# Kernel tuning notes

Hardware: AMD Instinct MI355X
Metric: run time of the kernel (lower is better)

The kernel has to match this reference:

```python
import jax, jax.numpy as jnp
import numpy as np

N_NODES = 100000

def setup_inputs() -> dict:
    key = jax.random.key(0)
    k1, k2, k3, k4 = jax.random.split(key, 4)
    feat = jax.random.normal(k1, (N_NODES, 256), dtype=jnp.float32)
    # xavier_uniform for [256,256]: bound = sqrt(6/(256+256))
    bound = float(np.sqrt(6.0 / (256 + 256)))
    weight1 = jax.random.uniform(k2, (256, 256), dtype=jnp.float32, minval=-bound, maxval=bound)
    src = jax.random.randint(k3, (1600000,), 0, N_NODES, dtype=jnp.int64)
    dst = jax.random.randint(k4, (1600000,), 0, N_NODES, dtype=jnp.int64)
    return {"feat": feat, "weight1": weight1, "src": src, "dst": dst}

def reference(feat, weight1, src, dst):
    # Per-etype copy_src + scatter-sum accumulated across etypes == one
    # segment_sum over the union of all edges (norm is computed but unused
    # in the original _apply).
    agg = jax.ops.segment_sum(feat[src], dst, num_segments=N_NODES)  # [N, d]
    h = (agg + feat) @ weight1
    h = jax.nn.relu(h)
    # F.dropout(training=False) is identity
    return h
```

## Files before the change

kernel.cpp:

```cpp
#include <hip/hip_runtime.h>

#define D 256
#define SCAN_THREADS 1024
#define CAP 32
#define MAXOVF 4096
#define BM 64

#define RN 32
#define RSH 5
#define SCAP 1024
#define PCH 8192
#define PTH 512
#define NRANGES_MAX 4096
#define SGT 256

typedef float f32x4 __attribute__((ext_vector_type(4)));
typedef short s16x8 __attribute__((ext_vector_type(8)));

__device__ inline unsigned int f2bf(float x) {
    unsigned int u = __float_as_uint(x);
    return (u + 0x7FFFu + ((u >> 16) & 1u)) >> 16;
}
__device__ inline float bflo(unsigned int u) { return __uint_as_float(u << 16); }
__device__ inline float bfhi(unsigned int u) { return __uint_as_float(u & 0xFFFF0000u); }

__global__ __launch_bounds__(256) void k_pre(const float* __restrict__ feat,
                                             unsigned short* __restrict__ featb,
                                             const float* __restrict__ W,
                                             unsigned short* __restrict__ wTs,
                                             int* __restrict__ gcur, int nz, long n8) {
    const int bid = blockIdx.x;
    const int t = threadIdx.x;
    if (bid < 256) {
        unsigned short v = (unsigned short)f2bf(W[(size_t)t * D + bid]);
        int ks = t >> 5;
        int byte = ((bid << 6) + (((t >> 3) & 3) << 4) + ((t & 7) << 1)) ^ ((bid & 7) << 4);
        *reinterpret_cast<unsigned short*>(
            reinterpret_cast<char*>(wTs) + (size_t)ks * 16384 + byte) = v;
    } else if (bid < 272) {
        int i = (bid - 256) * 256 + t;
        if (i < nz) gcur[i] = 0;
    }
    for (long i = bid * 256L + t; i < n8; i += (long)gridDim.x * 256) {
        const float4* p = reinterpret_cast<const float4*>(feat + i * 8);
        float4 a = p[0], b = p[1];
        uint4 u;
        u.x = f2bf(a.x) | (f2bf(a.y) << 16);
        u.y = f2bf(a.z) | (f2bf(a.w) << 16);
        u.z = f2bf(b.x) | (f2bf(b.y) << 16);
        u.w = f2bf(b.z) | (f2bf(b.w) << 16);
        reinterpret_cast<uint4*>(featb)[i] = u;
    }
}


__global__ void k_zero(int* __restrict__ p, int n) {
    int i = blockIdx.x * blockDim.x + threadIdx.x;
    if (i < n) p[i] = 0;
}

__global__ __launch_bounds__(256) void k_f2b(const float* __restrict__ f,
                                             unsigned short* __restrict__ fb, long n8) {
    for (long i = blockIdx.x * 256L + threadIdx.x; i < n8; i += (long)gridDim.x * 256) {
        const float4* p = reinterpret_cast<const float4*>(f + i * 8);
        float4 a = p[0], b = p[1];
        uint4 u;
        u.x = f2bf(a.x) | (f2bf(a.y) << 16);
        u.y = f2bf(a.z) | (f2bf(a.w) << 16);
        u.z = f2bf(b.x) | (f2bf(b.y) << 16);
        u.w = f2bf(b.z) | (f2bf(b.w) << 16);
        reinterpret_cast<uint4*>(fb)[i] = u;
    }
}

__global__ __launch_bounds__(256) void k_wTs(const float* __restrict__ W,
                                             unsigned short* __restrict__ wTs) {
    int col = blockIdx.x;
    int k = threadIdx.x;
    unsigned short v = (unsigned short)f2bf(W[(size_t)k * D + col]);
    int ks = k >> 5;
    int byte = ((col << 6) + (((k >> 3) & 3) << 4) + ((k & 7) << 1)) ^ ((col & 7) << 4);
    *reinterpret_cast<unsigned short*>(
        reinterpret_cast<char*>(wTs) + (size_t)ks * 16384 + byte) = v;
}

__global__ __launch_bounds__(PTH) void k_part(const int* __restrict__ src,
                                              const int* __restrict__ dst,
                                              int* __restrict__ gcur,
                                              int* __restrict__ streams,
                                              int* __restrict__ ovf,
                                              int* __restrict__ ovf_cnt,
                                              int E, int nranges) {
    __shared__ int hist[NRANGES_MAX];
    __shared__ int base[NRANGES_MAX];
    __shared__ int off[NRANGES_MAX];
    const int t = threadIdx.x;
    const long e0 = (long)blockIdx.x * PCH;
    for (int i = t; i < nranges; i += PTH) hist[i] = 0;
    __syncthreads();
    int md[PCH / PTH], ms[PCH / PTH];
    #pragma unroll
    for (int i = 0; i < PCH / PTH; ++i) {
        long e = e0 + (long)i * PTH + t;
        if (e < E) {
            md[i] = dst[e];
            ms[i] = src[e];
            atomicAdd(&hist[md[i] >> RSH], 1);
        } else {
            md[i] = -1;
        }
    }
    __syncthreads();
    for (int i = t; i < nranges; i += PTH) {
        int h = hist[i];
        base[i] = h ? atomicAdd(&gcur[i], h) : 0;
        off[i] = 0;
    }
    __syncthreads();
    #pragma unroll
    for (int i = 0; i < PCH / PTH; ++i) {
        if (md[i] >= 0) {
            int r = md[i] >> RSH;
            int p = base[r] + atomicAdd(&off[r], 1);
            if (p < SCAP) {
                streams[(size_t)r * SCAP + p] = (ms[i] << RSH) | (md[i] & (RN - 1));
            } else {
                int o = atomicAdd(ovf_cnt, 1);
                if (o < MAXOVF) { ovf[2 * o] = ms[i]; ovf[2 * o + 1] = md[i]; }
            }
        }
    }
}

__global__ __launch_bounds__(SGT) void k_sg(const unsigned short* __restrict__ featb,
                                            const int* __restrict__ gcur,
                                            const int* __restrict__ streams,
                                            const int* __restrict__ ovf,
                                            const int* __restrict__ ovf_cnt,
                                            unsigned short* __restrict__ aggb, int N) {
    __shared__ int hist[RN], basei[RN], off[RN], scn[RN];
    __shared__ int elist[SCAP];
    const int r = blockIdx.x;
    const int t = threadIdx.x;
    const int node0 = r << RSH;
    int cnt = gcur[r];
    if (cnt > SCAP) cnt = SCAP;
    if (t < RN) { hist[t] = 0; off[t] = 0; }
    __syncthreads();
    int ent[SCAP / SGT];
    #pragma unroll
    for (int i = 0; i < SCAP / SGT; ++i) {
        int p = t + i * SGT;
        if (p < cnt) {
            ent[i] = streams[(size_t)r * SCAP + p];
            atomicAdd(&hist[ent[i] & (RN - 1)], 1);
        } else {
            ent[i] = -1;
        }
    }
    __syncthreads();
    if (t < RN) scn[t] = hist[t];
    __syncthreads();
    for (int st = 1; st < RN; st <<= 1) {
        int v = 0;
        if (t < RN && t >= st) v = scn[t - st];
        __syncthreads();
        if (t < RN) scn[t] += v;
        __syncthreads();
    }
    if (t < RN) basei[t] = scn[t] - hist[t];
    __syncthreads();
    #pragma unroll
    for (int i = 0; i < SCAP / SGT; ++i) {
        if (ent[i] >= 0) {
            int ln_ = ent[i] & (RN - 1);
            int p = basei[ln_] + atomicAdd(&off[ln_], 1);
            elist[p] = ent[i] >> RSH;
        }
    }
    __syncthreads();
    int ovfn = *ovf_cnt;
    if (ovfn > MAXOVF) ovfn = MAXOVF;
    const int wv = t >> 6;
    const int l = t & 63;
    for (int k = 0; k < RN / 4; ++k) {
        int ln_ = wv * (RN / 4) + k;
        int node = node0 + ln_;
        if (node >= N) continue;
        int cb = hist[ln_];
        int bb = basei[ln_];
        uint2 u = reinterpret_cast<const uint2*>(featb + (size_t)node * D)[l];
        float4 acc;
        acc.x = bflo(u.x); acc.y = bfhi(u.x); acc.z = bflo(u.y); acc.w = bfhi(u.y);
        int j = 0;
        for (; j + 16 <= cb; j += 16) {
            int s[16];
            #pragma unroll
            for (int q = 0; q < 16; ++q) s[q] = elist[bb + j + q];
            uint2 v[16];
            #pragma unroll
            for (int q = 0; q < 16; ++q)
                v[q] = reinterpret_cast<const uint2*>(featb + (size_t)s[q] * D)[l];
            #pragma unroll
            for (int q = 0; q < 16; ++q) {
                acc.x += bflo(v[q].x); acc.y += bfhi(v[q].x);
                acc.z += bflo(v[q].y); acc.w += bfhi(v[q].y);
            }
        }
        for (; j + 8 <= cb; j += 8) {
            int s[8];
            #pragma unroll
            for (int q = 0; q < 8; ++q) s[q] = elist[bb + j + q];
            uint2 v[8];
            #pragma unroll
            for (int q = 0; q < 8; ++q)
                v[q] = reinterpret_cast<const uint2*>(featb + (size_t)s[q] * D)[l];
            #pragma unroll
            for (int q = 0; q < 8; ++q) {
                acc.x += bflo(v[q].x); acc.y += bfhi(v[q].x);
                acc.z += bflo(v[q].y); acc.w += bfhi(v[q].y);
            }
        }
        for (; j < cb; ++j) {
            uint2 v = reinterpret_cast<const uint2*>(featb + (size_t)elist[bb + j] * D)[l];
            acc.x += bflo(v.x); acc.y += bfhi(v.x);
            acc.z += bflo(v.y); acc.w += bfhi(v.y);
        }
        if (ovfn > 0) {
            for (int e = 0; e < ovfn; ++e) {
                if (ovf[2 * e + 1] == node) {
                    uint2 v = reinterpret_cast<const uint2*>(featb + (size_t)ovf[2 * e] * D)[l];
                    acc.x += bflo(v.x); acc.y += bfhi(v.x);
                    acc.z += bflo(v.y); acc.w += bfhi(v.y);
                }
            }
        }
        uint2 w;
        w.x = f2bf(acc.x) | (f2bf(acc.y) << 16);
        w.y = f2bf(acc.z) | (f2bf(acc.w) << 16);
        unsigned short* rowp = aggb + (size_t)node * D;
        int us = (l * 4) ^ ((node & 7) << 3);
        *reinterpret_cast<uint2*>(rowp + us) = w;
    }
}

__global__ void k_fillcap(const int* __restrict__ src, const int* __restrict__ dst,
                          int* __restrict__ counts, int* __restrict__ buckets,
                          int* __restrict__ ovf, int* __restrict__ ovf_cnt, int E) {
    for (int e = blockIdx.x * blockDim.x + threadIdx.x; e < E;
         e += gridDim.x * blockDim.x) {
        int d = dst[e];
        int pos = atomicAdd(&counts[d], 1);
        if (pos < CAP) {
            buckets[(size_t)d * CAP + pos] = src[e];
        } else {
            int o = atomicAdd(ovf_cnt, 1);
            if (o < MAXOVF) {
                ovf[2 * o + 0] = src[e];
                ovf[2 * o + 1] = d;
            }
        }
    }
}


#define GAT_BODY(LOAD, ACCUM)                                                  \
    int j = 0;                                                                 \
    for (; j + 16 <= cnt; j += 16) {                                           \
        int s[16];                                                             \
        _Pragma("unroll") for (int q = 0; q < 16; ++q) s[q] = bk[j + q];       \
        LOAD(16)                                                               \
        ACCUM(16)                                                              \
    }                                                                          \
    for (; j + 8 <= cnt; j += 8) {                                             \
        int s[8];                                                              \
        _Pragma("unroll") for (int q = 0; q < 8; ++q) s[q] = bk[j + q];        \
        LOAD(8)                                                                \
        ACCUM(8)                                                               \
    }

__global__ __launch_bounds__(256) void g_bf_aggb(const unsigned short* __restrict__ fb,
                                                 const int* __restrict__ counts,
                                                 const int* __restrict__ buckets,
                                                 const int* __restrict__ ovf,
                                                 const int* __restrict__ ovf_cnt,
                                                 unsigned short* __restrict__ aggb, int N) {
    int node = (int)((blockIdx.x * (long)blockDim.x + threadIdx.x) >> 6);
    int ln = threadIdx.x & 63;
    if (node >= N) return;
    int cnt_raw = counts[node];
    int cnt = cnt_raw > CAP ? CAP : cnt_raw;
    const int* bk = buckets + (size_t)node * CAP;
    uint2 u = reinterpret_cast<const uint2*>(fb + (size_t)node * D)[ln];
    float4 acc;
    acc.x = bflo(u.x); acc.y = bfhi(u.x); acc.z = bflo(u.y); acc.w = bfhi(u.y);
#define BLOAD(W_)                                                              \
    uint2 v[W_];                                                               \
    _Pragma("unroll") for (int q = 0; q < W_; ++q)                             \
        v[q] = reinterpret_cast<const uint2*>(fb + (size_t)s[q] * D)[ln];
#define BACC(W_)                                                               \
    _Pragma("unroll") for (int q = 0; q < W_; ++q) {                           \
        acc.x += bflo(v[q].x); acc.y += bfhi(v[q].x);                          \
        acc.z += bflo(v[q].y); acc.w += bfhi(v[q].y);                          \
    }
    GAT_BODY(BLOAD, BACC)
    for (; j < cnt; ++j) {
        uint2 v = reinterpret_cast<const uint2*>(fb + (size_t)bk[j] * D)[ln];
        acc.x += bflo(v.x); acc.y += bfhi(v.x);
        acc.z += bflo(v.y); acc.w += bfhi(v.y);
    }
    if (cnt_raw > CAP) {
        int m = *ovf_cnt;
        if (m > MAXOVF) m = MAXOVF;
        for (int e = 0; e < m; ++e) {
            if (ovf[2 * e + 1] == node) {
                uint2 v = reinterpret_cast<const uint2*>(fb + (size_t)ovf[2 * e] * D)[ln];
                acc.x += bflo(v.x); acc.y += bfhi(v.x);
                acc.z += bflo(v.y); acc.w += bfhi(v.y);
            }
        }
    }
    uint2 w;
    w.x = f2bf(acc.x) | (f2bf(acc.y) << 16);
    w.y = f2bf(acc.z) | (f2bf(acc.w) << 16);
    unsigned short* rowp = aggb + (size_t)node * D;
    int us = (ln * 4) ^ ((node & 7) << 3);
    *reinterpret_cast<uint2*>(rowp + us) = w;
}

__global__ __launch_bounds__(256) void g_f32_out(const float* __restrict__ feat,
                                                 const int* __restrict__ counts,
                                                 const int* __restrict__ buckets,
                                                 const int* __restrict__ ovf,
                                                 const int* __restrict__ ovf_cnt,
                                                 float* __restrict__ out, int N) {
    int node = (int)((blockIdx.x * (long)blockDim.x + threadIdx.x) >> 6);
    int ln = threadIdx.x & 63;
    if (node >= N) return;
    int cnt_raw = counts[node];
    int cnt = cnt_raw > CAP ? CAP : cnt_raw;
    const int* bk = buckets + (size_t)node * CAP;
    float4 acc = reinterpret_cast<const float4*>(feat + (size_t)node * D)[ln];
#define FLOAD(W_)                                                              \
    float4 v[W_];                                                              \
    _Pragma("unroll") for (int q = 0; q < W_; ++q)                             \
        v[q] = reinterpret_cast<const float4*>(feat + (size_t)s[q] * D)[ln];
#define FACC(W_)                                                               \
    _Pragma("unroll") for (int q = 0; q < W_; ++q) {                           \
        acc.x += v[q].x; acc.y += v[q].y; acc.z += v[q].z; acc.w += v[q].w;    \
    }
    GAT_BODY(FLOAD, FACC)
    for (; j < cnt; ++j) {
        float4 v = reinterpret_cast<const float4*>(feat + (size_t)bk[j] * D)[ln];
        acc.x += v.x; acc.y += v.y; acc.z += v.z; acc.w += v.w;
    }
    if (cnt_raw > CAP) {
        int m = *ovf_cnt;
        if (m > MAXOVF) m = MAXOVF;
        for (int e = 0; e < m; ++e) {
            if (ovf[2 * e + 1] == node) {
                float4 v = reinterpret_cast<const float4*>(feat + (size_t)ovf[2 * e] * D)[ln];
                acc.x += v.x; acc.y += v.y; acc.z += v.z; acc.w += v.w;
            }
        }
    }
    reinterpret_cast<float4*>(out + (size_t)node * D)[ln] = acc;
}


__global__ __launch_bounds__(256) void gc_copy(const float* __restrict__ feat,
                                               float* __restrict__ agg, long n4) {
    long i = (long)blockIdx.x * blockDim.x + threadIdx.x;
    if (i < n4)
        reinterpret_cast<float4*>(agg)[i] = reinterpret_cast<const float4*>(feat)[i];
}

__global__ __launch_bounds__(256) void gc_scatter(const float* __restrict__ feat,
                                                  const int* __restrict__ src,
                                                  const int* __restrict__ dst,
                                                  float* __restrict__ agg, int n_edges) {
    int wave = (int)((blockIdx.x * (long)blockDim.x + threadIdx.x) >> 6);
    int lane = threadIdx.x & 63;
    if (wave >= n_edges) return;
    int s = src[wave];
    int d = dst[wave];
    const float4 v = reinterpret_cast<const float4*>(feat + (size_t)s * D)[lane];
    float* p = agg + (size_t)d * D + (size_t)lane * 4;
    atomicAdd(p + 0, v.x);
    atomicAdd(p + 1, v.y);
    atomicAdd(p + 2, v.z);
    atomicAdd(p + 3, v.w);
}


__device__ inline void gload16(const char* g, const unsigned char* lds) {
    __builtin_amdgcn_global_load_lds(
        (const __attribute__((address_space(1))) void*)g,
        (__attribute__((address_space(3))) void*)lds, 16, 0, 0);
}

__global__ __launch_bounds__(256) void gemm_mfma_b(const unsigned short* __restrict__ aggb,
                                                   const unsigned short* __restrict__ wTs,
                                                   float* __restrict__ out, int n_rows) {
    __shared__ __align__(16) unsigned char s_a[BM * 512];
    __shared__ __align__(16) unsigned char s_b[16384];
    const int t = threadIdx.x;
    const int row0 = blockIdx.x * BM;
    const int wv = t >> 6;
    const int l = t & 63;
    const char* wb = reinterpret_cast<const char*>(wTs);

    const char* gbase = reinterpret_cast<const char*>(aggb) + (size_t)row0 * 512;
    #pragma unroll
    for (int q = 0; q < 8; ++q) {
        int off = wv * 8192 + q * 1024;
        gload16(gbase + off + l * 16, s_a + off);
    }
    #pragma unroll
    for (int i = 0; i < 4; ++i) {
        int off = wv * 4096 + i * 1024;
        gload16(wb + off + l * 16, s_b + off);
    }
    __syncthreads();

    f32x4 acc[16];
    #pragma unroll
    for (int ct = 0; ct < 16; ++ct) acc[ct] = (f32x4){0.f, 0.f, 0.f, 0.f};

    const int lr = wv * 16 + (l & 15);
    const int g = l >> 4;
    for (int ks = 0; ks < 8; ++ks) {
        const int kb = ks * 32 + g * 8;
        const int ab = (lr * 512 + kb * 2) ^ ((lr & 7) << 4);
        s16x8 af = *reinterpret_cast<const s16x8*>(s_a + ab);
        #pragma unroll
        for (int ct = 0; ct < 16; ++ct) {
            int col = ct * 16 + (l & 15);
            int bb = (col * 64 + g * 16) ^ ((col & 7) << 4);
            s16x8 bf = *reinterpret_cast<const s16x8*>(s_b + bb);
            acc[ct] = __builtin_amdgcn_mfma_f32_16x16x32_bf16(af, bf, acc[ct], 0, 0, 0);
        }
        __syncthreads();
        if (ks < 7) {
            #pragma unroll
            for (int i = 0; i < 4; ++i) {
                int off = wv * 4096 + i * 1024;
                gload16(wb + (size_t)(ks + 1) * 16384 + off + l * 16, s_b + off);
            }
            __syncthreads();
        }
    }

    const int rbase = row0 + wv * 16 + (l >> 4) * 4;
    const int cb = l & 15;
    #pragma unroll
    for (int ct = 0; ct < 16; ++ct) {
        #pragma unroll
        for (int r = 0; r < 4; ++r) {
            int row = rbase + r;
            if (row < n_rows)
                out[(size_t)row * D + ct * 16 + cb] = fmaxf(acc[ct][r], 0.f);
        }
    }
}

__global__ __launch_bounds__(256) void gemm_mfma(const unsigned short* __restrict__ wTs,
                                                 float* __restrict__ out, int n_rows) {
    __shared__ __align__(16) unsigned char s_a[BM * 512];
    __shared__ __align__(16) unsigned char s_b[16384];
    const int t = threadIdx.x;
    const int row0 = blockIdx.x * BM;
    const int wv = t >> 6;
    const int l = t & 63;
    const char* wb = reinterpret_cast<const char*>(wTs);

    #pragma unroll
    for (int i = 0; i < 4; ++i) {
        int off = wv * 4096 + i * 1024;
        gload16(wb + off + l * 16, s_b + off);
    }
    #pragma unroll
    for (int i = 0; i < 16; ++i) {
        int f4 = t + 256 * i;
        int row = f4 >> 6;
        int kc = f4 & 63;
        int grow = row0 + row;
        if (grow >= n_rows) grow = n_rows - 1;
        float4 v = *reinterpret_cast<const float4*>(out + (size_t)grow * D + kc * 4);
        uint2 u;
        u.x = f2bf(v.x) | (f2bf(v.y) << 16);
        u.y = f2bf(v.z) | (f2bf(v.w) << 16);
        int byte = (row * 512 + kc * 8) ^ ((row & 7) << 4);
        *reinterpret_cast<uint2*>(s_a + byte) = u;
    }
    __syncthreads();

    f32x4 acc[16];
    #pragma unroll
    for (int ct = 0; ct < 16; ++ct) acc[ct] = (f32x4){0.f, 0.f, 0.f, 0.f};

    const int lr = wv * 16 + (l & 15);
    const int g = l >> 4;
    for (int ks = 0; ks < 8; ++ks) {
        const int kb = ks * 32 + g * 8;
        const int ab = (lr * 512 + kb * 2) ^ ((lr & 7) << 4);
        s16x8 af = *reinterpret_cast<const s16x8*>(s_a + ab);
        #pragma unroll
        for (int ct = 0; ct < 16; ++ct) {
            int col = ct * 16 + (l & 15);
            int bb = (col * 64 + g * 16) ^ ((col & 7) << 4);
            s16x8 bf = *reinterpret_cast<const s16x8*>(s_b + bb);
            acc[ct] = __builtin_amdgcn_mfma_f32_16x16x32_bf16(af, bf, acc[ct], 0, 0, 0);
        }
        __syncthreads();
        if (ks < 7) {
            #pragma unroll
            for (int i = 0; i < 4; ++i) {
                int off = wv * 4096 + i * 1024;
                gload16(wb + (size_t)(ks + 1) * 16384 + off + l * 16, s_b + off);
            }
            __syncthreads();
        }
    }

    const int rbase = row0 + wv * 16 + (l >> 4) * 4;
    const int cb = l & 15;
    #pragma unroll
    for (int ct = 0; ct < 16; ++ct) {
        #pragma unroll
        for (int r = 0; r < 4; ++r) {
            int row = rbase + r;
            if (row < n_rows)
                out[(size_t)row * D + ct * 16 + cb] = fmaxf(acc[ct][r], 0.f);
        }
    }
}

__global__ __launch_bounds__(256) void gemm_relu(const float* __restrict__ Wm,
                                                 float* __restrict__ out, int n_rows) {
    __shared__ float s_a[32][D];
    const int row0 = blockIdx.x * 32;
    const int c = threadIdx.x;
    {
        const float4* gsrc = reinterpret_cast<const float4*>(out + (size_t)row0 * D);
        float4* ldst = reinterpret_cast<float4*>(&s_a[0][0]);
        #pragma unroll
        for (int i = 0; i < 8; ++i)
            ldst[threadIdx.x + i * 256] = gsrc[threadIdx.x + i * 256];
    }
    __syncthreads();
    float acc[32];
    #pragma unroll
    for (int r = 0; r < 32; ++r) acc[r] = 0.f;
    #pragma unroll 4
    for (int k = 0; k < D; ++k) {
        float w = Wm[(size_t)k * D + c];
        #pragma unroll
        for (int r = 0; r < 32; ++r) acc[r] += s_a[r][k] * w;
    }
    #pragma unroll
    for (int r = 0; r < 32; ++r) {
        int row = row0 + r;
        if (row < n_rows) out[(size_t)row * D + c] = fmaxf(acc[r], 0.f);
    }
}

extern "C" void kernel_launch(void* const* d_in, const int* in_sizes, int n_in,
                              void* d_out, int out_size, void* d_ws, size_t ws_size,
                              hipStream_t stream) {
    const float* feat = (const float*)d_in[0];
    const float* W    = (const float*)d_in[1];
    const int*   src  = (const int*)d_in[2];
    const int*   dst  = (const int*)d_in[3];
    float* out = (float*)d_out;

    const int N = in_sizes[0] / D;
    const int E = in_sizes[2];
    const int Npad = ((N + BM - 1) / BM) * BM;
    auto al = [](size_t x) { return (x + 255) & ~(size_t)255; };

    const int nranges = (N + RN - 1) / RN;
    const int gemm_blocks = (N + BM - 1) / BM;
    const int gat_blocks = (N + 3) / 4;

    const size_t hdr_bytes   = ((size_t)nranges + 1 + 2 * MAXOVF) * 4;
    const size_t strm_off    = al(hdr_bytes);
    const size_t strm_sz     = (size_t)nranges * SCAP * 4;
    const size_t a2_featb_off = al(strm_off + strm_sz);
    const size_t featb_sz    = (size_t)N * D * 2;
    const size_t a2_wt_off   = al(a2_featb_off + featb_sz);
    const size_t wt_sz       = (size_t)D * D * 2;
    const size_t a2_aggb_off = al(a2_wt_off + wt_sz);
    const size_t aggb_sz     = (size_t)Npad * D * 2;
    const size_t need_A2     = a2_aggb_off + aggb_sz;

    const size_t cap_bytes = ((size_t)N + 1 + 2 * MAXOVF + (size_t)N * CAP) * 4;
    const size_t featb_off = al(cap_bytes);
    const size_t wt_off    = al(featb_off + featb_sz);
    const size_t aggb_off  = al(wt_off + wt_sz);
    const size_t need_A    = aggb_off + aggb_sz;

    if (ws_size >= need_A2 && nranges <= NRANGES_MAX) {
        char* base = (char*)d_ws;
        int* gcur    = (int*)base;
        int* ovf_cnt = gcur + nranges;
        int* ovf     = ovf_cnt + 1;
        int* streams = (int*)(base + strm_off);
        unsigned short* featb = (unsigned short*)(base + a2_featb_off);
        unsigned short* wTs   = (unsigned short*)(base + a2_wt_off);
        unsigned short* aggb  = (unsigned short*)(base + a2_aggb_off);

        k_pre<<<2048, 256, 0, stream>>>(feat, featb, W, wTs, gcur, nranges + 1,
                                        (long)N * D / 8);
        k_part<<<(E + PCH - 1) / PCH, PTH, 0, stream>>>(src, dst, gcur, streams,
                                                        ovf, ovf_cnt, E, nranges);
        k_sg<<<nranges, SGT, 0, stream>>>(featb, gcur, streams, ovf, ovf_cnt, aggb, N);
        gemm_mfma_b<<<gemm_blocks, 256, 0, stream>>>(aggb, wTs, out, N);
    } else if (ws_size >= need_A) {
        char* base = (char*)d_ws;
        int* counts  = (int*)base;
        int* ovf_cnt = counts + N;
        int* ovf     = ovf_cnt + 1;
        int* buckets = ovf + 2 * MAXOVF;
        unsigned short* featb = (unsigned short*)(base + featb_off);
        unsigned short* wTs   = (unsigned short*)(base + wt_off);
        unsigned short* aggb  = (unsigned short*)(base + aggb_off);

        k_zero<<<(N + 1 + 255) / 256, 256, 0, stream>>>(counts, N + 1);
        k_f2b<<<2048, 256, 0, stream>>>(feat, featb, (long)N * D / 8);
        k_wTs<<<D, 256, 0, stream>>>(W, wTs);
        k_fillcap<<<2048, 256, 0, stream>>>(src, dst, counts, buckets, ovf, ovf_cnt, E);
        g_bf_aggb<<<gat_blocks, 256, 0, stream>>>(featb, counts, buckets, ovf, ovf_cnt, aggb, N);
        gemm_mfma_b<<<gemm_blocks, 256, 0, stream>>>(aggb, wTs, out, N);
    } else if (ws_size >= cap_bytes) {
        char* base = (char*)d_ws;
        int* counts  = (int*)base;
        int* ovf_cnt = counts + N;
        int* ovf     = ovf_cnt + 1;
        int* buckets = ovf + 2 * MAXOVF;
        unsigned short* wTs = (unsigned short*)(((uintptr_t)buckets + 255) & ~(uintptr_t)255);

        k_zero<<<(N + 1 + 255) / 256, 256, 0, stream>>>(counts, N + 1);
        k_fillcap<<<2048, 256, 0, stream>>>(src, dst, counts, buckets, ovf, ovf_cnt, E);
        g_f32_out<<<gat_blocks, 256, 0, stream>>>(feat, counts, buckets, ovf, ovf_cnt, out, N);
        k_wTs<<<D, 256, 0, stream>>>(W, wTs);
        gemm_mfma<<<gemm_blocks, 256, 0, stream>>>(wTs, out, N);
    } else {
        long n4 = (long)N * D / 4;
        gc_copy<<<(int)((n4 + 255) / 256), 256, 0, stream>>>(feat, out, n4);
        gc_scatter<<<(E + 3) / 4, 256, 0, stream>>>(feat, src, dst, out, E);
        gemm_relu<<<(N + 31) / 32, 256, 0, stream>>>(W, out, N);
    }
}
```

Before: 231.1 us.

## Fuse segment-gather aggregation with bf16 MFMA GEMM and ReLU epilogue

The gather kernel no longer writes the aggregated bf16 rows to global memory for a separate GEMM kernel. Each block keeps its 32 aggregated rows in LDS, streams the transposed weight slices into LDS with global_load_lds, and runs MFMA 16x16x32 bf16 to write the ReLU output directly. This removes the aggb round trip and one kernel launch. In exchange, every block reloads the full 128KB weight matrix for only 32 rows, uses more LDS per block (lower occupancy), and adds barriers in the K loop with no double buffering.

```diff
diff --git a/kernel.cpp b/kernel.cpp
--- a/kernel.cpp
+++ b/kernel.cpp
@@ -1,7 +1,6 @@
 #include <hip/hip_runtime.h>
 
 #define D 256
-#define SCAN_THREADS 1024
 #define CAP 32
 #define MAXOVF 4096
 #define BM 64
@@ -23,6 +22,12 @@
 }
 __device__ inline float bflo(unsigned int u) { return __uint_as_float(u << 16); }
 __device__ inline float bfhi(unsigned int u) { return __uint_as_float(u & 0xFFFF0000u); }
+
+__device__ inline void gload16(const char* g, const unsigned char* lds) {
+    __builtin_amdgcn_global_load_lds(
+        (const __attribute__((address_space(1))) void*)g,
+        (__attribute__((address_space(3))) void*)lds, 16, 0, 0);
+}
 
 __global__ __launch_bounds__(256) void k_pre(const float* __restrict__ feat,
                                              unsigned short* __restrict__ featb,
@@ -132,17 +137,30 @@
     }
 }
 
-__global__ __launch_bounds__(SGT) void k_sg(const unsigned short* __restrict__ featb,
-                                            const int* __restrict__ gcur,
-                                            const int* __restrict__ streams,
-                                            const int* __restrict__ ovf,
-                                            const int* __restrict__ ovf_cnt,
-                                            unsigned short* __restrict__ aggb, int N) {
+__global__ __launch_bounds__(SGT) void k_sgg(const unsigned short* __restrict__ featb,
+                                             const int* __restrict__ gcur,
+                                             const int* __restrict__ streams,
+                                             const int* __restrict__ ovf,
+                                             const int* __restrict__ ovf_cnt,
+                                             const unsigned short* __restrict__ wTs,
+                                             float* __restrict__ out, int N) {
     __shared__ int hist[RN], basei[RN], off[RN], scn[RN];
     __shared__ int elist[SCAP];
+    __shared__ __align__(16) unsigned char s_agg[RN * 512];
+    __shared__ __align__(16) unsigned char s_b[16384];
     const int r = blockIdx.x;
     const int t = threadIdx.x;
     const int node0 = r << RSH;
+    const int wv = t >> 6;
+    const int l = t & 63;
+    const char* wb = reinterpret_cast<const char*>(wTs);
+
+    #pragma unroll
+    for (int i = 0; i < 4; ++i) {
+        int o = wv * 4096 + i * 1024;
+        gload16(wb + o + l * 16, s_b + o);
+    }
+
     int cnt = gcur[r];
     if (cnt > SCAP) cnt = SCAP;
     if (t < RN) { hist[t] = 0; off[t] = 0; }
@@ -179,14 +197,19 @@
         }
     }
     __syncthreads();
+
     int ovfn = *ovf_cnt;
     if (ovfn > MAXOVF) ovfn = MAXOVF;
-    const int wv = t >> 6;
-    const int l = t & 63;
     for (int k = 0; k < RN / 4; ++k) {
         int ln_ = wv * (RN / 4) + k;
         int node = node0 + ln_;
-        if (node >= N) continue;
+        unsigned short* rowp = reinterpret_cast<unsigned short*>(s_agg) + ln_ * 256;
+        int us = (l * 4) ^ ((ln_ & 7) << 3);
+        if (node >= N) {
+            uint2 z; z.x = 0; z.y = 0;
+            *reinterpret_cast<uint2*>(rowp + us) = z;
+            continue;
+        }
         int cb = hist[ln_];
         int bb = basei[ln_];
         uint2 u = reinterpret_cast<const uint2*>(featb + (size_t)node * D)[l];
@@ -238,9 +261,58 @@
         uint2 w;
         w.x = f2bf(acc.x) | (f2bf(acc.y) << 16);
         w.y = f2bf(acc.z) | (f2bf(acc.w) << 16);
-        unsigned short* rowp = aggb + (size_t)node * D;
-        int us = (l * 4) ^ ((node & 7) << 3);
         *reinterpret_cast<uint2*>(rowp + us) = w;
+    }
+    __syncthreads();
+
+    f32x4 acc[2][4];
+    #pragma unroll
+    for (int rt = 0; rt < 2; ++rt)
+        #pragma unroll
+        for (int ct = 0; ct < 4; ++ct) acc[rt][ct] = (f32x4){0.f, 0.f, 0.f, 0.f};
+
+    const int g = l >> 4;
+    const int cl = l & 15;
+    for (int ks = 0; ks < 8; ++ks) {
+        const int kb = ks * 32 + g * 8;
+        s16x8 af[2];
+        #pragma unroll
+        for (int rt = 0; rt < 2; ++rt) {
+            int lr = rt * 16 + cl;
+            int ab = (lr * 512 + kb * 2) ^ ((lr & 7) << 4);
+            af[rt] = *reinterpret_cast<const s16x8*>(s_agg + ab);
+        }
+        #pragma unroll
+        for (int ct = 0; ct < 4; ++ct) {
+            int col = wv * 64 + ct * 16 + cl;
+            int bb = (col * 64 + g * 16) ^ ((col & 7) << 4);
+            s16x8 bf = *reinterpret_cast<const s16x8*>(s_b + bb);
+            acc[0][ct] = __builtin_amdgcn_mfma_f32_16x16x32_bf16(af[0], bf, acc[0][ct], 0, 0, 0);
+            acc[1][ct] = __builtin_amdgcn_mfma_f32_16x16x32_bf16(af[1], bf, acc[1][ct], 0, 0, 0);
+        }
+        __syncthreads();
+        if (ks < 7) {
+            #pragma unroll
+            for (int i = 0; i < 4; ++i) {
+                int o = wv * 4096 + i * 1024;
+                gload16(wb + (size_t)(ks + 1) * 16384 + o + l * 16, s_b + o);
+            }
+            __syncthreads();
+        }
+    }
+
+    #pragma unroll
+    for (int rt = 0; rt < 2; ++rt) {
+        #pragma unroll
+        for (int ct = 0; ct < 4; ++ct) {
+            #pragma unroll
+            for (int rr = 0; rr < 4; ++rr) {
+                int row = node0 + rt * 16 + (l >> 4) * 4 + rr;
+                int col = wv * 64 + ct * 16 + cl;
+                if (row < N)
+                    out[(size_t)row * D + col] = fmaxf(acc[rt][ct][rr], 0.f);
+            }
+        }
     }
 }
 
@@ -393,12 +465,6 @@
 }
 
 
-__device__ inline void gload16(const char* g, const unsigned char* lds) {
-    __builtin_amdgcn_global_load_lds(
-        (const __attribute__((address_space(1))) void*)g,
-        (__attribute__((address_space(3))) void*)lds, 16, 0, 0);
-}
-
 __global__ __launch_bounds__(256) void gemm_mfma_b(const unsigned short* __restrict__ aggb,
                                                    const unsigned short* __restrict__ wTs,
                                                    float* __restrict__ out, int n_rows) {
@@ -590,14 +656,13 @@
     const size_t featb_sz    = (size_t)N * D * 2;
     const size_t a2_wt_off   = al(a2_featb_off + featb_sz);
     const size_t wt_sz       = (size_t)D * D * 2;
-    const size_t a2_aggb_off = al(a2_wt_off + wt_sz);
-    const size_t aggb_sz     = (size_t)Npad * D * 2;
-    const size_t need_A2     = a2_aggb_off + aggb_sz;
+    const size_t need_A2     = a2_wt_off + wt_sz;
 
     const size_t cap_bytes = ((size_t)N + 1 + 2 * MAXOVF + (size_t)N * CAP) * 4;
     const size_t featb_off = al(cap_bytes);
     const size_t wt_off    = al(featb_off + featb_sz);
     const size_t aggb_off  = al(wt_off + wt_sz);
+    const size_t aggb_sz   = (size_t)Npad * D * 2;
     const size_t need_A    = aggb_off + aggb_sz;
 
     if (ws_size >= need_A2 && nranges <= NRANGES_MAX) {
@@ -608,14 +673,13 @@
         int* streams = (int*)(base + strm_off);
         unsigned short* featb = (unsigned short*)(base + a2_featb_off);
         unsigned short* wTs   = (unsigned short*)(base + a2_wt_off);
-        unsigned short* aggb  = (unsigned short*)(base + a2_aggb_off);
 
         k_pre<<<2048, 256, 0, stream>>>(feat, featb, W, wTs, gcur, nranges + 1,
                                         (long)N * D / 8);
         k_part<<<(E + PCH - 1) / PCH, PTH, 0, stream>>>(src, dst, gcur, streams,
                                                         ovf, ovf_cnt, E, nranges);
-        k_sg<<<nranges, SGT, 0, stream>>>(featb, gcur, streams, ovf, ovf_cnt, aggb, N);
-        gemm_mfma_b<<<gemm_blocks, 256, 0, stream>>>(aggb, wTs, out, N);
+        k_sgg<<<nranges, SGT, 0, stream>>>(featb, gcur, streams, ovf, ovf_cnt,
+                                           wTs, out, N);
     } else if (ws_size >= need_A) {
         char* base = (char*)d_ws;
         int* counts  = (int*)base;
```

Result: faster. 215.3 us (-6.8%).
